# Kernel tuning notes

Hardware: AMD Instinct MI355X
Metric: run time of the kernel (lower is better)

The kernel has to match this reference:

```python
import jax, jax.numpy as jnp
import numpy as np

N_STREAMS = 8
D_MODEL = 2048
S_EXP = 2
NS = N_STREAMS * S_EXP            # 16
N_SKEW = NS * (NS - 1) // 2       # 120
B, L = 2, 4096

# static upper-triangular index pairs (constants)
_TRIU_R, _TRIU_C = np.triu_indices(NS, k=1)
TRIU_R = jnp.asarray(_TRIU_R)
TRIU_C = jnp.asarray(_TRIU_C)


def setup_inputs() -> dict:
    key = jax.random.key(0)
    k1, k2, k3 = jax.random.split(key, 3)
    streams = jax.random.normal(k1, (B, L, N_STREAMS, D_MODEL), dtype=jnp.float32)
    # W_res: torch Linear weight layout [out_features, in_features]; small init
    # (the module zero-inits, but we use random weights for a meaningful test)
    W = jax.random.normal(k2, (N_SKEW, D_MODEL), dtype=jnp.float32) * 0.02
    b = jax.random.normal(k3, (N_SKEW,), dtype=jnp.float32) * 0.02
    return {"streams": streams, "W": W, "b": b}


def reference(streams, W, b):
    # streams: [B, L, n, d]
    x_agg = streams.mean(axis=2)                      # [B, L, d]
    z = jnp.einsum('bld,kd->blk', x_agg, W) + b       # [B, L, n_skew]
    # build skew-symmetric A: upper triangle = z, lower = -z
    Bq, Lq = z.shape[0], z.shape[1]
    S = jnp.zeros((Bq, Lq, NS, NS), dtype=z.dtype).at[..., TRIU_R, TRIU_C].set(z)
    A = S - jnp.swapaxes(S, -1, -2)                   # [B, L, ns, ns]
    I = jnp.eye(NS, dtype=z.dtype)
    # Cayley transform: Q = (I + A)^{-1} (I - A)  in SO(ns)
    Q = jnp.linalg.solve(I + A, I - A)                # [B, L, ns, ns]
    # block Frobenius norms -> exactly doubly stochastic H_res
    Qb = Q.reshape(Bq, Lq, N_STREAMS, S_EXP, N_STREAMS, S_EXP)
    H_res = (Qb ** 2).sum(axis=(3, 5)) / S_EXP        # [B, L, n, n]
    return H_res
```

## Files before the change

### kernel.cpp

```cpp
#include <hip/hip_runtime.h>

#define NSTR 8
#define DM 2048
#define NK 120
#define NKP 128


__global__ __launch_bounds__(256)
void mean8(const float4* __restrict__ s4, float4* __restrict__ xa4, int pbase) {
    const size_t idx = (size_t)blockIdx.x * 256 + threadIdx.x;
    const size_t p = idx >> 9;
    const int d4 = (int)(idx & 511);
    const float4* src = s4 + ((size_t)(pbase) + p) * (NSTR * DM / 4) + d4;
    float4 v = src[0];
#pragma unroll
    for (int n = 1; n < 8; ++n) {
        const float4 u = src[(size_t)n * (DM / 4)];
        v.x += u.x; v.y += u.y; v.z += u.z; v.w += u.w;
    }
    v.x *= 0.125f; v.y *= 0.125f; v.z *= 0.125f; v.w *= 0.125f;
    xa4[idx] = v;
}

__global__ __launch_bounds__(256, 2)
void proj(const float* __restrict__ xa, const float* __restrict__ Wm,
          float* __restrict__ zp, int npos) {
    __shared__ float4 sxa[128 * 16];
    __shared__ float4 sw[128 * 16];

    const int t = threadIdx.x;
    const int slice = blockIdx.x & 7;
    const int ptile = blockIdx.x >> 3;
    const int pos0 = ptile * 128;
    const int typ = t >> 4;
    const int txk = t & 15;
    const int c = t & 15;
    const int rbase = t >> 4;

    float4 ra[8], rw[8];
    float acc[8][8];
#pragma unroll
    for (int i = 0; i < 8; ++i)
#pragma unroll
        for (int j = 0; j < 8; ++j) acc[i][j] = 0.f;

    {
        const int ds0 = slice * 256;
#pragma unroll
        for (int r = 0; r < 8; ++r) {
            const int p = rbase + 16 * r;
            ra[r] = *(const float4*)(xa + (size_t)(pos0 + p) * DM + ds0 + c * 4);
        }
#pragma unroll
        for (int r = 0; r < 8; ++r) {
            const int k = rbase + 16 * r;
            rw[r] = (k < NK) ? *(const float4*)(Wm + (size_t)k * DM + ds0 + c * 4)
                             : make_float4(0.f, 0.f, 0.f, 0.f);
        }
    }

#pragma unroll 1
    for (int sub = 0; sub < 4; ++sub) {
#pragma unroll
        for (int r = 0; r < 8; ++r) {
            const int p = rbase + 16 * r;
            sxa[p * 16 + (c ^ (p >> 3))] = ra[r];
        }
#pragma unroll
        for (int r = 0; r < 8; ++r) {
            const int k = rbase + 16 * r;
            sw[k * 16 + (c ^ (k >> 3))] = rw[r];
        }
        __syncthreads();

        if (sub < 3) {
            const int ds0 = slice * 256 + (sub + 1) * 64;
#pragma unroll
            for (int r = 0; r < 8; ++r) {
                const int p = rbase + 16 * r;
                ra[r] = *(const float4*)(xa + (size_t)(pos0 + p) * DM + ds0 + c * 4);
            }
#pragma unroll
            for (int r = 0; r < 8; ++r) {
                const int k = rbase + 16 * r;
                rw[r] = (k < NK) ? *(const float4*)(Wm + (size_t)k * DM + ds0 + c * 4)
                                 : make_float4(0.f, 0.f, 0.f, 0.f);
            }
        }

        for (int dq = 0; dq < 16; ++dq) {
            float4 a[8];
#pragma unroll
            for (int i = 0; i < 8; ++i) a[i] = sxa[(typ * 8 + i) * 16 + (dq ^ typ)];
#pragma unroll
            for (int j = 0; j < 8; ++j) {
                const float4 bv = sw[(txk * 8 + j) * 16 + (dq ^ txk)];
#pragma unroll
                for (int i = 0; i < 8; ++i) {
                    acc[i][j] = fmaf(a[i].x, bv.x, acc[i][j]);
                    acc[i][j] = fmaf(a[i].y, bv.y, acc[i][j]);
                    acc[i][j] = fmaf(a[i].z, bv.z, acc[i][j]);
                    acc[i][j] = fmaf(a[i].w, bv.w, acc[i][j]);
                }
            }
        }
        __syncthreads();
    }

    float* base = zp + (size_t)slice * npos * NKP;
#pragma unroll
    for (int i = 0; i < 8; ++i) {
        float* dst = base + (size_t)(pos0 + typ * 8 + i) * NKP + txk * 8;
        *(float4*)dst = make_float4(acc[i][0], acc[i][1], acc[i][2], acc[i][3]);
        *((float4*)dst + 1) = make_float4(acc[i][4], acc[i][5], acc[i][6], acc[i][7]);
    }
}

template <int NPARTS>
__global__ __launch_bounds__(256)
void cayley_k(const float* __restrict__ zb, long long zstride,
              const float* __restrict__ bvec, float* __restrict__ out, int pbase) {
    const int t = threadIdx.x;
    const int wave = t >> 6;
    const int l = t & 63;
    const int pos = blockIdx.x * 4 + wave;
    const int j = l & 15;
    const int g = l >> 4;

    float m[4], x[4];
#pragma unroll
    for (int r = 0; r < 4; ++r) {
        const int i = 4 * r + g;
        float a;
        if (i != j) {
            int k;
            float sgn;
            if (i < j) { k = (i * (31 - i)) / 2 + (j - i - 1); sgn = 1.f; }
            else       { k = (j * (31 - j)) / 2 + (i - j - 1); sgn = -1.f; }
            const size_t off = (size_t)pos * NKP + k;
            float zv = zb[off];
#pragma unroll
            for (int s = 1; s < NPARTS; ++s) zv += zb[off + (size_t)s * zstride];
            a = sgn * (zv + bvec[k]);
        } else {
            a = 0.f;
        }
        const float d = (i == j) ? 1.f : 0.f;
        m[r] = d + a;
        x[r] = d - a;
    }

#pragma unroll
    for (int k = 0; k < 16; ++k) {
        const int rr = k >> 2;
        const int src_row = (k & 3) << 4;
        const float mk  = __shfl(m[rr], src_row | j, 64);
        const float xk  = __shfl(x[rr], src_row | j, 64);
        const float mkk = __shfl(m[rr], src_row | k, 64);
        const float rk = 1.0f / mkk;
#pragma unroll
        for (int r = 0; r < 4; ++r) {
            const float mik = __shfl(m[r], (g << 4) | k, 64);
            const float f = (4 * r + g == k) ? 0.f : mik * rk;
            m[r] = fmaf(-f, mk, m[r]);
            x[r] = fmaf(-f, xk, x[r]);
        }
    }

    float h[4];
#pragma unroll
    for (int r = 0; r < 4; ++r) {
        const int i = 4 * r + g;
        const float mdiag = __shfl(m[r], (g << 4) | i, 64);
        const float q = x[r] / mdiag;
        float s = q * q;
        s += __shfl_xor(s, 1, 64);
        s += __shfl_xor(s, 16, 64);
        h[r] = s * 0.5f;
    }
    if (((j & 1) == 0) && ((g & 1) == 0)) {
        const int col = j >> 1;
#pragma unroll
        for (int r = 0; r < 4; ++r) {
            const int row = 2 * r + (g >> 1);
            out[(size_t)(pbase + pos) * 64 + row * 8 + col] = h[r];
        }
    }
}

#define TM 128
#define DSLICE 256
#define SD 64

__global__ void zero_ws(float4* z4) {
    z4[(size_t)blockIdx.x * 256 + threadIdx.x] = make_float4(0.f, 0.f, 0.f, 0.f);
}

__global__ __launch_bounds__(256, 2)
void mean_proj_fused(const float* __restrict__ streams, const float* __restrict__ W,
                     float* __restrict__ z) {
    __shared__ float4 sxa[TM * 16];
    __shared__ float4 sw[NKP * 16];

    const int t = threadIdx.x;
    const int bid = blockIdx.x;
    const int slice = bid >> 6;
    const int ptile = bid & 63;
    const int pos0 = ptile * TM;
    const int typ = t >> 4;
    const int txk = t & 15;

    float acc[8][8];
#pragma unroll
    for (int i = 0; i < 8; ++i)
#pragma unroll
        for (int j = 0; j < 8; ++j) acc[i][j] = 0.f;

    for (int sub = 0; sub < 4; ++sub) {
        const int ds0 = slice * DSLICE + sub * SD;
#pragma unroll
        for (int r = 0; r < 8; ++r) {
            const int item = t + 256 * r;
            const int p = item >> 4;
            const int dq = item & 15;
            const float4* src = (const float4*)(streams
                + (size_t)(pos0 + p) * NSTR * DM + ds0 + dq * 4);
            float4 v = src[0];
#pragma unroll
            for (int n = 1; n < 8; ++n) {
                const float4 u = src[n * (DM / 4)];
                v.x += u.x; v.y += u.y; v.z += u.z; v.w += u.w;
            }
            v.x *= 0.125f; v.y *= 0.125f; v.z *= 0.125f; v.w *= 0.125f;
            sxa[p * 16 + (dq ^ (p >> 3))] = v;
        }
#pragma unroll
        for (int r = 0; r < 8; ++r) {
            const int item = t + 256 * r;
            const int k = item >> 4;
            const int dq = item & 15;
            float4 v = make_float4(0.f, 0.f, 0.f, 0.f);
            if (k < NK) v = *(const float4*)(W + (size_t)k * DM + ds0 + dq * 4);
            sw[k * 16 + (dq ^ (k >> 3))] = v;
        }
        __syncthreads();

        for (int dq = 0; dq < 16; ++dq) {
            float4 a[8];
#pragma unroll
            for (int i = 0; i < 8; ++i) a[i] = sxa[(typ * 8 + i) * 16 + (dq ^ typ)];
#pragma unroll
            for (int j = 0; j < 8; ++j) {
                const float4 bv = sw[(txk * 8 + j) * 16 + (dq ^ txk)];
#pragma unroll
                for (int i = 0; i < 8; ++i) {
                    acc[i][j] = fmaf(a[i].x, bv.x, acc[i][j]);
                    acc[i][j] = fmaf(a[i].y, bv.y, acc[i][j]);
                    acc[i][j] = fmaf(a[i].z, bv.z, acc[i][j]);
                    acc[i][j] = fmaf(a[i].w, bv.w, acc[i][j]);
                }
            }
        }
        __syncthreads();
    }

#pragma unroll
    for (int i = 0; i < 8; ++i) {
        const size_t p = (size_t)pos0 + typ * 8 + i;
#pragma unroll
        for (int j = 0; j < 8; ++j) {
            const int k = txk * 8 + j;
            if (k < NK) atomicAdd(&z[p * NKP + k], acc[i][j]);
        }
    }
}

extern "C" void kernel_launch(void* const* d_in, const int* in_sizes, int n_in,
                              void* d_out, int out_size, void* d_ws, size_t ws_size,
                              hipStream_t stream) {
    const float* streams = (const float*)d_in[0];
    const float* W       = (const float*)d_in[1];
    const float* bvec    = (const float*)d_in[2];
    float* out = (float*)d_out;

    const size_t TOTPOS = 8192;
    const size_t XA_FULL = TOTPOS * DM * sizeof(float);
    const size_t ZP_FULL = 8 * TOTPOS * NKP * sizeof(float);

    int nb = 0;
    size_t npos = 0;
    if (ws_size >= XA_FULL + ZP_FULL)               { nb = 1; npos = 8192; }
    else if (ws_size >= (XA_FULL + ZP_FULL) / 2)    { nb = 2; npos = 4096; }

    if (nb > 0) {
        float* xa = (float*)d_ws;
        float* zp = (float*)((char*)d_ws + npos * DM * sizeof(float));
        const long long zstride = (long long)npos * NKP;
        for (int b = 0; b < nb; ++b) {
            const int pbase = (int)(b * npos);
            mean8<<<(int)(npos * 2), 256, 0, stream>>>(
                (const float4*)streams, (float4*)xa, pbase);
            proj<<<(int)((npos / 128) * 8), 256, 0, stream>>>(xa, W, zp, (int)npos);
            cayley_k<8><<<(int)(npos / 4), 256, 0, stream>>>(zp, zstride, bvec, out, pbase);
        }
    } else {
        float* z = (float*)d_ws;
        zero_ws<<<1024, 256, 0, stream>>>((float4*)d_ws);
        mean_proj_fused<<<512, 256, 0, stream>>>(streams, W, z);
        cayley_k<1><<<2048, 256, 0, stream>>>(z, 0, bvec, out, 0);
    }
}
```

Before: 778.5 us.

## Interleave projection partials per position and coalesce the Cayley input reduction

The projection kernel now writes its 8 slice partials next to each other for each position instead of in separate slice planes. The Cayley kernel reads those partials as contiguous float4 loads, sums them with a cross-lane shuffle, adds the bias and stages the 120 coefficients in shared memory. This replaces the earlier scattered per-element gathers across 8 strided planes. The mean kernel is also changed to one block per position with two float4 loads per thread per stream. The cost is an extra block-wide barrier and some shared memory in the Cayley kernel.

```diff
diff --git a/kernel.cpp b/kernel.cpp
--- a/kernel.cpp
+++ b/kernel.cpp
@@ -8,18 +8,22 @@
 
 __global__ __launch_bounds__(256)
 void mean8(const float4* __restrict__ s4, float4* __restrict__ xa4, int pbase) {
-    const size_t idx = (size_t)blockIdx.x * 256 + threadIdx.x;
-    const size_t p = idx >> 9;
-    const int d4 = (int)(idx & 511);
-    const float4* src = s4 + ((size_t)(pbase) + p) * (NSTR * DM / 4) + d4;
-    float4 v = src[0];
+    const int t = threadIdx.x;
+    const size_t p = blockIdx.x;
+    const float4* src = s4 + (size_t)(pbase + p) * (NSTR * DM / 4);
+    float4 a = src[t];
+    float4 b = src[t + 256];
 #pragma unroll
     for (int n = 1; n < 8; ++n) {
-        const float4 u = src[(size_t)n * (DM / 4)];
-        v.x += u.x; v.y += u.y; v.z += u.z; v.w += u.w;
-    }
-    v.x *= 0.125f; v.y *= 0.125f; v.z *= 0.125f; v.w *= 0.125f;
-    xa4[idx] = v;
+        const float4 u = src[(size_t)n * (DM / 4) + t];
+        const float4 w = src[(size_t)n * (DM / 4) + t + 256];
+        a.x += u.x; a.y += u.y; a.z += u.z; a.w += u.w;
+        b.x += w.x; b.y += w.y; b.z += w.z; b.w += w.w;
+    }
+    a.x *= 0.125f; a.y *= 0.125f; a.z *= 0.125f; a.w *= 0.125f;
+    b.x *= 0.125f; b.y *= 0.125f; b.z *= 0.125f; b.w *= 0.125f;
+    xa4[p * (DM / 4) + t] = a;
+    xa4[p * (DM / 4) + t + 256] = b;
 }
 
 __global__ __launch_bounds__(256, 2)
@@ -107,10 +111,9 @@
         __syncthreads();
     }
 
-    float* base = zp + (size_t)slice * npos * NKP;
 #pragma unroll
     for (int i = 0; i < 8; ++i) {
-        float* dst = base + (size_t)(pos0 + typ * 8 + i) * NKP + txk * 8;
+        float* dst = zp + ((size_t)(pos0 + typ * 8 + i) * 8 + slice) * NKP + txk * 8;
         *(float4*)dst = make_float4(acc[i][0], acc[i][1], acc[i][2], acc[i][3]);
         *((float4*)dst + 1) = make_float4(acc[i][4], acc[i][5], acc[i][6], acc[i][7]);
     }
@@ -118,8 +121,9 @@
 
 template <int NPARTS>
 __global__ __launch_bounds__(256)
-void cayley_k(const float* __restrict__ zb, long long zstride,
-              const float* __restrict__ bvec, float* __restrict__ out, int pbase) {
+void cayley_k(const float* __restrict__ zp, const float* __restrict__ bvec,
+              float* __restrict__ out, int pbase) {
+    __shared__ float zrow[4][NKP];
     const int t = threadIdx.x;
     const int wave = t >> 6;
     const int l = t & 63;
@@ -127,21 +131,40 @@
     const int j = l & 15;
     const int g = l >> 4;
 
+    {
+        const float4* src = (const float4*)(zp + (size_t)pos * NPARTS * NKP);
+        float4 s = make_float4(0.f, 0.f, 0.f, 0.f);
+#pragma unroll
+        for (int q = 0; q < (NPARTS + 1) / 2; ++q) {
+            const int idx = l + 64 * q;
+            if (idx < NPARTS * 32) {
+                const float4 v = src[idx];
+                s.x += v.x; s.y += v.y; s.z += v.z; s.w += v.w;
+            }
+        }
+        s.x += __shfl_xor(s.x, 32, 64);
+        s.y += __shfl_xor(s.y, 32, 64);
+        s.z += __shfl_xor(s.z, 32, 64);
+        s.w += __shfl_xor(s.w, 32, 64);
+        if (l < 32) {
+            if (l < 30) {
+                const float4 b4 = ((const float4*)bvec)[l];
+                s.x += b4.x; s.y += b4.y; s.z += b4.z; s.w += b4.w;
+            }
+            ((float4*)&zrow[wave][0])[l] = s;
+        }
+    }
+    __syncthreads();
+
     float m[4], x[4];
 #pragma unroll
     for (int r = 0; r < 4; ++r) {
         const int i = 4 * r + g;
         float a;
-        if (i != j) {
-            int k;
-            float sgn;
-            if (i < j) { k = (i * (31 - i)) / 2 + (j - i - 1); sgn = 1.f; }
-            else       { k = (j * (31 - j)) / 2 + (i - j - 1); sgn = -1.f; }
-            const size_t off = (size_t)pos * NKP + k;
-            float zv = zb[off];
-#pragma unroll
-            for (int s = 1; s < NPARTS; ++s) zv += zb[off + (size_t)s * zstride];
-            a = sgn * (zv + bvec[k]);
+        if (i < j) {
+            a = zrow[wave][(i * (31 - i)) / 2 + (j - i - 1)];
+        } else if (i > j) {
+            a = -zrow[wave][(j * (31 - j)) / 2 + (i - j - 1)];
         } else {
             a = 0.f;
         }
@@ -295,18 +318,17 @@
     if (nb > 0) {
         float* xa = (float*)d_ws;
         float* zp = (float*)((char*)d_ws + npos * DM * sizeof(float));
-        const long long zstride = (long long)npos * NKP;
         for (int b = 0; b < nb; ++b) {
             const int pbase = (int)(b * npos);
-            mean8<<<(int)(npos * 2), 256, 0, stream>>>(
+            mean8<<<(int)npos, 256, 0, stream>>>(
                 (const float4*)streams, (float4*)xa, pbase);
             proj<<<(int)((npos / 128) * 8), 256, 0, stream>>>(xa, W, zp, (int)npos);
-            cayley_k<8><<<(int)(npos / 4), 256, 0, stream>>>(zp, zstride, bvec, out, pbase);
+            cayley_k<8><<<(int)(npos / 4), 256, 0, stream>>>(zp, bvec, out, pbase);
         }
     } else {
         float* z = (float*)d_ws;
         zero_ws<<<1024, 256, 0, stream>>>((float4*)d_ws);
         mean_proj_fused<<<512, 256, 0, stream>>>(streams, W, z);
-        cayley_k<1><<<2048, 256, 0, stream>>>(z, 0, bvec, out, 0);
-    }
-}
+        cayley_k<1><<<2048, 256, 0, stream>>>(z, bvec, out, 0);
+    }
+}
```

New measurement: 780.8 us. About the same (+0.3%).
